# Kernel tuning notes

Hardware: AMD Instinct MI355X
Metric: run time of the kernel (lower is better)

The kernel has to match this reference:

```python
import jax, jax.numpy as jnp
import numpy as np

H = 16  # heads

def setup_inputs() -> dict:
    key = jax.random.key(0)
    k1, k2, k3 = jax.random.split(key, 3)
    B, N, D = 2, 2048, 1024
    x = jax.random.normal(k1, (B, N, D), dtype=jnp.float32)
    W1 = jax.random.normal(k2, (D, 3 * D), dtype=jnp.float32) * (1.0 / np.sqrt(D))
    b1 = jnp.zeros((3 * D,), dtype=jnp.float32)
    W2 = jax.random.normal(k3, (D, D), dtype=jnp.float32) * (1.0 / np.sqrt(D))
    b2 = jnp.zeros((D,), dtype=jnp.float32)
    return {"x": x, "W1": W1, "b1": b1, "W2": W2, "b2": b2}

def reference(x, W1, b1, W2, b2):
    B, N, D = x.shape
    Dh = D // H  # head dim
    qkv = x @ W1 + b1                         # [B,N,3D]
    q, k, v = jnp.split(qkv, 3, axis=-1)
    q = q.reshape(B, N, H, Dh).transpose(0, 2, 1, 3)  # [B,H,N,Dh]
    k = k.reshape(B, N, H, Dh).transpose(0, 2, 1, 3)
    v = v.reshape(B, N, H, Dh).transpose(0, 2, 1, 3)
    scale = 1.0 / np.sqrt(Dh)
    w = jnp.einsum('bhnd,bhmd->bhnm', q, k) * scale   # [B,H,N,N]
    w = jax.nn.softmax(w, axis=-1)
    out = jnp.einsum('bhnm,bhmd->bhnd', w, v)         # [B,H,N,Dh]
    out = out.transpose(0, 2, 1, 3).reshape(B, N, D)
    return out @ W2 + b2
```

## Files before the change

kernel.cpp:

```cpp
#include <hip/hip_runtime.h>
#include <hip/hip_bf16.h>
#include <stdint.h>

#define B_   2
#define H_   16
#define N_   2048
#define D_   1024
#define DH   64
#define MTOK 4096

#define LOG2E 1.44269504088896f

typedef __attribute__((ext_vector_type(8)))  short bf16x8;
typedef __attribute__((ext_vector_type(4)))  float f32x4;
typedef __attribute__((ext_vector_type(16))) float f32x16;
typedef __attribute__((ext_vector_type(2)))  unsigned u32x2;
typedef __attribute__((ext_vector_type(4)))  unsigned short us4;

#define VMCNT_ASM(N) asm volatile("s_waitcnt vmcnt(" #N ")" ::: "memory")

static __device__ __forceinline__ unsigned short f2bf(float f) {
    union { float f; unsigned u; } v; v.f = f;
    unsigned r = v.u + 0x7fffu + ((v.u >> 16) & 1u);
    return (unsigned short)(r >> 16);
}

static __device__ __forceinline__ unsigned f2u(float x) {
    union { float f; unsigned u; } v; v.f = x; return v.u;
}
static __device__ __forceinline__ float u2f(unsigned x) {
    union { unsigned u; float f; } v; v.u = x; return v.f;
}

static __device__ __forceinline__ unsigned cvt_pk_bf16(float lo, float hi) {
    unsigned r;
    asm("v_cvt_pk_bf16_f32 %0, %1, %2" : "=v"(r) : "v"(lo), "v"(hi));
    return r;
}

static __device__ __forceinline__ bf16x8 frag_from_u32(unsigned a, unsigned b, unsigned c, unsigned d) {
    union { unsigned u[4]; bf16x8 v; } x;
    x.u[0] = a; x.u[1] = b; x.u[2] = c; x.u[3] = d;
    return x.v;
}

static __device__ __forceinline__ void load_lds16(const void* g, void* l) {
    __builtin_amdgcn_global_load_lds(
        (const __attribute__((address_space(1))) unsigned int*)g,
        (__attribute__((address_space(3))) unsigned int*)l, 16, 0, 0);
}

__global__ __launch_bounds__(256) void k_cvt_x(const float* __restrict__ x,
                                               unsigned short* __restrict__ xb, int n) {
    int idx = (blockIdx.x * 256 + threadIdx.x) * 4;
    if (idx < n) {
        float4 v = *(const float4*)(x + idx);
        us4 o;
        o.x = f2bf(v.x); o.y = f2bf(v.y); o.z = f2bf(v.z); o.w = f2bf(v.w);
        *(us4*)(xb + idx) = o;
    }
}

__global__ __launch_bounds__(256) void k_transpose_w(const float* __restrict__ in,
                                                     unsigned short* __restrict__ out,
                                                     int R, int C) {
    __shared__ float tile[64][65];
    int c0 = blockIdx.x * 64, r0 = blockIdx.y * 64;
    int t = threadIdx.x;
    int tr = t >> 4, tc = (t & 15) * 4;
#pragma unroll
    for (int p = 0; p < 4; p++) {
        int row = p * 16 + tr;
        float4 v = *(const float4*)(in + (size_t)(r0 + row) * C + c0 + tc);
        tile[row][tc + 0] = v.x; tile[row][tc + 1] = v.y;
        tile[row][tc + 2] = v.z; tile[row][tc + 3] = v.w;
    }
    __syncthreads();
    int oc = t >> 4, orr = (t & 15) * 4;
#pragma unroll
    for (int p = 0; p < 4; p++) {
        int crow = p * 16 + oc;
        us4 o;
        o.x = f2bf(tile[orr + 0][crow]);
        o.y = f2bf(tile[orr + 1][crow]);
        o.z = f2bf(tile[orr + 2][crow]);
        o.w = f2bf(tile[orr + 3][crow]);
        *(us4*)(out + (size_t)(c0 + crow) * R + r0 + orr) = o;
    }
}

__global__ __launch_bounds__(512, 2) void k_gemm0(const unsigned short* __restrict__ A,
                                                  const unsigned short* __restrict__ Bt,
                                                  const float* __restrict__ bias,
                                                  unsigned short* __restrict__ qdst,
                                                  unsigned short* __restrict__ kdst,
                                                  unsigned short* __restrict__ vdst) {
    __shared__ unsigned short lds[57344];
    const int K = 1024, NT = 16;
    int tid = threadIdx.x;
    int lane = tid & 63, wv = tid >> 6;
    int wm = wv >> 2, wn = wv & 3;
    int F = blockIdx.x;
    int L = (F & 7) * 32 + (F >> 3);
    int n0 = (L % 16) * 192;
    int m0 = (L / 16) * 256;

    f32x4 acc[8][3];
#pragma unroll
    for (int i = 0; i < 8; i++)
#pragma unroll
        for (int j = 0; j < 3; j++) {
            f32x4 z; z[0] = 0.f; z[1] = 0.f; z[2] = 0.f; z[3] = 0.f;
            acc[i][j] = z;
        }

    auto stage = [&](int t) {
        int p = t & 1;
        int k0 = t * 64;
        unsigned short* ab = &lds[p * 16384];
        unsigned short* bb = &lds[32768 + p * 12288];
#pragma unroll
        for (int i = 0; i < 4; i++) {
            int u = i * 512 + tid;
            int r = u >> 3, c8 = u & 7;
            int c8s = c8 ^ ((r & 4) ? 2 : 0);
            int db = (i * 512 + wv * 64) * 8;
            load_lds16(A + (size_t)(m0 + r) * K + k0 + c8s * 8, &ab[db]);
            if (i < 3)
                load_lds16(Bt + (size_t)(n0 + r) * K + k0 + c8s * 8, &bb[db]);
        }
    };

    stage(0);
    stage(1);

    const int ml = lane & 15, kl = (lane >> 4) * 8;
    const int cswz = (lane & 4) ? 16 : 0;
    bf16x8 afr[4], bfr[3];

#pragma unroll 1
    for (int t = 0; t < NT; ++t) {
        if (t < NT - 1) { VMCNT_ASM(7); }
        else            { VMCNT_ASM(0); }
        __builtin_amdgcn_s_barrier();

        const unsigned short* ab = &lds[(t & 1) * 16384];
        const unsigned short* bb = &lds[32768 + (t & 1) * 12288];

#pragma unroll
        for (int kk = 0; kk < 2; ++kk) {
            int ck = (kk * 32 + kl) ^ cswz;
#pragma unroll
            for (int mh = 0; mh < 2; ++mh) {
                if (mh == 0) {
#pragma unroll
                    for (int nj = 0; nj < 3; nj++)
                        bfr[nj] = *(const bf16x8*)&bb[(wn * 48 + nj * 16 + ml) * 64 + ck];
                }
#pragma unroll
                for (int q = 0; q < 4; q++)
                    afr[q] = *(const bf16x8*)&ab[(wm * 128 + (mh * 4 + q) * 16 + ml) * 64 + ck];
                __builtin_amdgcn_s_barrier();
                __builtin_amdgcn_s_setprio(1);
#pragma unroll
                for (int q = 0; q < 4; q++)
#pragma unroll
                    for (int nj = 0; nj < 3; nj++)
                        acc[mh * 4 + q][nj] = __builtin_amdgcn_mfma_f32_16x16x32_bf16(
                            afr[q], bfr[nj], acc[mh * 4 + q][nj], 0, 0, 0);
                __builtin_amdgcn_s_setprio(0);
                __builtin_amdgcn_s_barrier();
            }
        }
        if (t + 2 < NT) stage(t + 2);
    }

#pragma unroll
    for (int nj = 0; nj < 3; nj++) {
        int col = n0 + wn * 48 + nj * 16 + (lane & 15);
        float bv = bias[col];
        int which = col >> 10;
        int hd = (col >> 6) & 15;
        int dh = col & 63;
        float scl = (which == 0) ? (0.125f * LOG2E) : 1.0f;
#pragma unroll
        for (int mi = 0; mi < 8; mi++) {
            int rbase = m0 + wm * 128 + mi * 16 + (lane >> 4) * 4;
#pragma unroll
            for (int r = 0; r < 4; r++) {
                int tok = rbase + r;
                int bb2 = tok >> 11, nn = tok & 2047;
                float vvv = (acc[mi][nj][r] + bv) * scl;
                size_t chunk = ((size_t)(bb2 * H_ + hd) * 64 + (nn >> 5)) * 2048;
                if (which == 0) {
                    qdst[((size_t)(bb2 * H_ + hd) * N_ + nn) * DH + dh] = f2bf(vvv);
                } else if (which == 1) {
                    int lane2 = ((dh >> 3) & 1) * 32 + (nn & 31);
                    kdst[chunk + (dh >> 4) * 512 + lane2 * 8 + (dh & 7)] = f2bf(vvv);
                } else {
                    int lane2 = ((nn >> 3) & 1) * 32 + (dh & 31);
                    int islot = (dh >> 5) * 2 + ((nn >> 4) & 1);
                    vdst[chunk + islot * 512 + lane2 * 8 + (nn & 7)] = f2bf(vvv);
                }
            }
        }
    }
}

__global__ __launch_bounds__(256) void k_gemm1(const unsigned short* __restrict__ A,
                                               const unsigned short* __restrict__ Bt,
                                               const float* __restrict__ bias,
                                               float* __restrict__ outp) {
    __shared__ unsigned short As[3][128 * 32];
    __shared__ unsigned short Bs[3][128 * 32];
    const int K = 1024;
    const int NT = 32;
    int tid = threadIdx.x;
    int lane = tid & 63, wv = tid >> 6;
    int wm = wv >> 1, wn = wv & 1;

    const int NX = 8, CPX = 32;
    int F = blockIdx.x;
    int L = (F & 7) * CPX + (F >> 3);
    int n0 = (L % NX) * 128;
    int m0 = (L / NX) * 128;
    int bIdx = m0 >> 11;
    int ntok0 = m0 & 2047;

    f32x4 acc[4][4];
#pragma unroll
    for (int i = 0; i < 4; i++)
#pragma unroll
        for (int j = 0; j < 4; j++) {
            f32x4 z; z[0] = 0.f; z[1] = 0.f; z[2] = 0.f; z[3] = 0.f;
            acc[i][j] = z;
        }

    auto stage = [&](int buf, int tt) {
        int k0 = tt * 32;
        int hh = k0 >> 6;
        const unsigned short* aptr = A + ((size_t)(bIdx * H_ + hh) * N_ + ntok0) * DH + (k0 & 63);
        const unsigned short* bptr = Bt + (size_t)n0 * K + k0;
#pragma unroll
        for (int i = 0; i < 2; i++) {
            int cidb = i * 256 + wv * 64;
            int cid = cidb + lane;
            int row = cid >> 2;
            int cg  = (cid & 3) ^ (row & 3);
            load_lds16(aptr + (size_t)row * DH + cg * 8, &As[buf][cidb * 8]);
            load_lds16(bptr + (size_t)row * K  + cg * 8, &Bs[buf][cidb * 8]);
        }
    };

    stage(0, 0);
    stage(1, 1);

    const int swz = ((lane >> 4) ^ (lane & 3)) * 8;
    const int ar0 = (wm * 64 + (lane & 15)) * 32 + swz;
    const int br0 = (wn * 64 + (lane & 15)) * 32 + swz;

#pragma unroll 1
    for (int t = 0; t < NT; ++t) {
        int cur = t % 3;
        if (t <= NT - 3) stage((t + 2) % 3, t + 2);
        if (t <= NT - 3)      { VMCNT_ASM(8); }
        else if (t == NT - 2) { VMCNT_ASM(4); }
        else                  { VMCNT_ASM(0); }
        __builtin_amdgcn_s_barrier();
        __builtin_amdgcn_sched_barrier(0);

        bf16x8 af[4], bfr[4];
#pragma unroll
        for (int mi = 0; mi < 4; mi++)
            af[mi] = *(const bf16x8*)&As[cur][ar0 + mi * 16 * 32];
#pragma unroll
        for (int ni = 0; ni < 4; ni++)
            bfr[ni] = *(const bf16x8*)&Bs[cur][br0 + ni * 16 * 32];
#pragma unroll
        for (int mi = 0; mi < 4; mi++)
#pragma unroll
            for (int ni = 0; ni < 4; ni++)
                acc[mi][ni] = __builtin_amdgcn_mfma_f32_16x16x32_bf16(
                    af[mi], bfr[ni], acc[mi][ni], 0, 0, 0);

        __builtin_amdgcn_s_barrier();
    }

#pragma unroll
    for (int ni = 0; ni < 4; ni++) {
        int col = n0 + wn * 64 + ni * 16 + (lane & 15);
        float bv = bias[col];
#pragma unroll
        for (int mi = 0; mi < 4; mi++) {
            int rbase = m0 + wm * 64 + mi * 16 + (lane >> 4) * 4;
#pragma unroll
            for (int r = 0; r < 4; r++)
                outp[(size_t)(rbase + r) * D_ + col] = acc[mi][ni][r] + bv;
        }
    }
}

__global__ __launch_bounds__(512, 2) void k_attn(const unsigned short* __restrict__ qh,
                                                 const unsigned short* __restrict__ ks,
                                                 const unsigned short* __restrict__ vs,
                                                 unsigned short* __restrict__ o) {
    __shared__ unsigned short smem[32768];
    unsigned short* kb = smem;
    unsigned short* vb = smem + 16384;
    float* red = (float*)smem;

    int tid = threadIdx.x;
    int lane = tid & 63, wv = tid >> 6;
    int qsub = wv >> 1;
    int kvh  = wv & 1;
    int F = blockIdx.x;
    int L = (F & 7) * 64 + (F >> 3);
    int bh = L >> 4;
    int q0 = (L & 15) * 128 + qsub * 32;
    int ln = lane & 31, hi = lane >> 5;
    const size_t bhO = (size_t)bh * N_ * DH;

    const unsigned short* qp = qh + bhO;
    bf16x8 qf[4];
#pragma unroll
    for (int kk = 0; kk < 4; kk++)
        qf[kk] = *(const bf16x8*)(qp + (size_t)(q0 + ln) * DH + kk * 16 + hi * 8);

    const unsigned short* kg = ks + (size_t)bh * 131072;
    const unsigned short* vg = vs + (size_t)bh * 131072;

    int sbuf = wv >> 1;
    int sl   = wv & 1;
    int sh   = sbuf & 1;
    unsigned short* dstb = ((sbuf >> 1) ? vb : kb) + sh * 8192 + sl * 2048;
    const unsigned short* srcb = ((sbuf >> 1) ? vg : kg) + (size_t)sh * 65536 + sl * 2048;
    auto stageT = [&](int ring, int t) {
#pragma unroll
        for (int i = 0; i < 4; i++)
            load_lds16(srcb + (size_t)t * 4096 + i * 512 + lane * 8,
                       dstb + ring * 4096 + i * 512);
    };

    f32x16 o0, o1;
#pragma unroll
    for (int r = 0; r < 16; r++) { o0[r] = 0.f; o1[r] = 0.f; }
    float m = -INFINITY, l = 0.f;

    stageT(0, 0);
    __syncthreads();

#pragma unroll 1
    for (int t = 0; t < 16; ++t) {
        int b = t & 1;
        if (t < 15) stageT(b ^ 1, t + 1);

        const unsigned short* kB = kb + kvh * 8192 + b * 4096;
        const unsigned short* vB = vb + kvh * 8192 + b * 4096;

        bf16x8 kfa[4], kfb[4];
#pragma unroll
        for (int i = 0; i < 4; i++) {
            kfa[i] = *(const bf16x8*)&kB[i * 512 + lane * 8];
            kfb[i] = *(const bf16x8*)&kB[2048 + i * 512 + lane * 8];
        }
        f32x16 sa, sb;
#pragma unroll
        for (int r = 0; r < 16; r++) { sa[r] = 0.f; sb[r] = 0.f; }
#pragma unroll
        for (int i = 0; i < 4; i++)
            sa = __builtin_amdgcn_mfma_f32_32x32x16_bf16(kfa[i], qf[i], sa, 0, 0, 0);
#pragma unroll
        for (int i = 0; i < 4; i++)
            sb = __builtin_amdgcn_mfma_f32_32x32x16_bf16(kfb[i], qf[i], sb, 0, 0, 0);

        float mx[8];
#pragma unroll
        for (int i = 0; i < 8; i++)
            mx[i] = fmaxf(fmaxf(sa[i], sa[i + 8]), fmaxf(sb[i], sb[i + 8]));
#pragma unroll
        for (int i = 0; i < 4; i++) mx[i] = fmaxf(mx[i], mx[i + 4]);
        float mt = fmaxf(fmaxf(mx[0], mx[2]), fmaxf(mx[1], mx[3]));
        {
            u32x2 sw = __builtin_amdgcn_permlane32_swap(f2u(mt), f2u(mt), false, false);
            mt = fmaxf(u2f(sw[0]), u2f(sw[1]));
        }
        if (!__all(mt <= m + 8.0f)) {
            float mn = fmaxf(m, mt);
            float fs = __builtin_amdgcn_exp2f(m - mn);
            m = mn;
            l *= fs;
#pragma unroll
            for (int r = 0; r < 16; r++) { o0[r] *= fs; o1[r] *= fs; }
        }
        float pa[16], pb[16];
#pragma unroll
        for (int r = 0; r < 16; r++) {
            pa[r] = __builtin_amdgcn_exp2f(sa[r] - m);
            pb[r] = __builtin_amdgcn_exp2f(sb[r] - m);
        }
        float sm[8];
#pragma unroll
        for (int i = 0; i < 8; i++) sm[i] = (pa[i] + pa[i + 8]) + (pb[i] + pb[i + 8]);
#pragma unroll
        for (int i = 0; i < 4; i++) sm[i] = sm[i] + sm[i + 4];
        float sum = (sm[0] + sm[2]) + (sm[1] + sm[3]);
        {
            u32x2 sw = __builtin_amdgcn_permlane32_swap(f2u(sum), f2u(sum), false, false);
            sum = u2f(sw[0]) + u2f(sw[1]);
        }
        l += sum;

        unsigned pka[8], pkb[8];
#pragma unroll
        for (int i = 0; i < 8; i++) {
            pka[i] = cvt_pk_bf16(pa[2 * i], pa[2 * i + 1]);
            pkb[i] = cvt_pk_bf16(pb[2 * i], pb[2 * i + 1]);
        }
        u32x2 s0 = __builtin_amdgcn_permlane32_swap(pka[0], pka[2], false, false);
        u32x2 s1 = __builtin_amdgcn_permlane32_swap(pka[1], pka[3], false, false);
        u32x2 s2 = __builtin_amdgcn_permlane32_swap(pka[4], pka[6], false, false);
        u32x2 s3 = __builtin_amdgcn_permlane32_swap(pka[5], pka[7], false, false);
        bf16x8 pf0 = frag_from_u32(s0[0], s1[0], s0[1], s1[1]);
        bf16x8 pf1 = frag_from_u32(s2[0], s3[0], s2[1], s3[1]);
        s0 = __builtin_amdgcn_permlane32_swap(pkb[0], pkb[2], false, false);
        s1 = __builtin_amdgcn_permlane32_swap(pkb[1], pkb[3], false, false);
        s2 = __builtin_amdgcn_permlane32_swap(pkb[4], pkb[6], false, false);
        s3 = __builtin_amdgcn_permlane32_swap(pkb[5], pkb[7], false, false);
        bf16x8 pf2 = frag_from_u32(s0[0], s1[0], s0[1], s1[1]);
        bf16x8 pf3 = frag_from_u32(s2[0], s3[0], s2[1], s3[1]);

        bf16x8 vf0, vf1, vf2, vf3;
        vf0 = *(const bf16x8*)&vB[0 * 512 + lane * 8];
        vf1 = *(const bf16x8*)&vB[1 * 512 + lane * 8];
        vf2 = *(const bf16x8*)&vB[2048 + 0 * 512 + lane * 8];
        vf3 = *(const bf16x8*)&vB[2048 + 1 * 512 + lane * 8];
        o0 = __builtin_amdgcn_mfma_f32_32x32x16_bf16(vf0, pf0, o0, 0, 0, 0);
        o0 = __builtin_amdgcn_mfma_f32_32x32x16_bf16(vf1, pf1, o0, 0, 0, 0);
        o0 = __builtin_amdgcn_mfma_f32_32x32x16_bf16(vf2, pf2, o0, 0, 0, 0);
        o0 = __builtin_amdgcn_mfma_f32_32x32x16_bf16(vf3, pf3, o0, 0, 0, 0);
        vf0 = *(const bf16x8*)&vB[2 * 512 + lane * 8];
        vf1 = *(const bf16x8*)&vB[3 * 512 + lane * 8];
        vf2 = *(const bf16x8*)&vB[2048 + 2 * 512 + lane * 8];
        vf3 = *(const bf16x8*)&vB[2048 + 3 * 512 + lane * 8];
        o1 = __builtin_amdgcn_mfma_f32_32x32x16_bf16(vf0, pf0, o1, 0, 0, 0);
        o1 = __builtin_amdgcn_mfma_f32_32x32x16_bf16(vf1, pf1, o1, 0, 0, 0);
        o1 = __builtin_amdgcn_mfma_f32_32x32x16_bf16(vf2, pf2, o1, 0, 0, 0);
        o1 = __builtin_amdgcn_mfma_f32_32x32x16_bf16(vf3, pf3, o1, 0, 0, 0);

        __syncthreads();
    }

    if (kvh == 1) {
        float* rp = red + (qsub * 64 + lane) * 34;
#pragma unroll
        for (int r = 0; r < 16; r++) { rp[r] = o0[r]; rp[16 + r] = o1[r]; }
        rp[32] = m;
        rp[33] = l;
    }
    __syncthreads();
    if (kvh == 0) {
        const float* rp = red + (qsub * 64 + lane) * 34;
        float mb = rp[32], lb = rp[33];
        float mn = fmaxf(m, mb);
        float fa = __builtin_amdgcn_exp2f(m - mn);
        float fb = __builtin_amdgcn_exp2f(mb - mn);
        float inv = 1.0f / (l * fa + lb * fb);
        float ga = fa * inv, gb = fb * inv;
        unsigned short* ob = o + bhO + (size_t)(q0 + ln) * DH;
#pragma unroll
        for (int t2 = 0; t2 < 2; t2++) {
#pragma unroll
            for (int g = 0; g < 4; g++) {
                int d = t2 * 32 + g * 8 + hi * 4;
                int rb = g * 4;
                float a0 = (t2 ? o1[rb + 0] : o0[rb + 0]) * ga + rp[t2 * 16 + rb + 0] * gb;
                float a1 = (t2 ? o1[rb + 1] : o0[rb + 1]) * ga + rp[t2 * 16 + rb + 1] * gb;
                float a2 = (t2 ? o1[rb + 2] : o0[rb + 2]) * ga + rp[t2 * 16 + rb + 2] * gb;
                float a3 = (t2 ? o1[rb + 3] : o0[rb + 3]) * ga + rp[t2 * 16 + rb + 3] * gb;
                us4 w;
                w.x = f2bf(a0); w.y = f2bf(a1); w.z = f2bf(a2); w.w = f2bf(a3);
                *(us4*)(ob + d) = w;
            }
        }
    }
}

extern "C" void kernel_launch(void* const* d_in, const int* in_sizes, int n_in,
                              void* d_out, int out_size, void* d_ws, size_t ws_size,
                              hipStream_t stream) {
    const float* x  = (const float*)d_in[0];
    const float* W1 = (const float*)d_in[1];
    const float* b1 = (const float*)d_in[2];
    const float* W2 = (const float*)d_in[3];
    const float* b2 = (const float*)d_in[4];
    float* out = (float*)d_out;

    char* ws = (char*)d_ws;
    unsigned short* xb   = (unsigned short*)(ws);
    unsigned short* w1t  = (unsigned short*)(ws + 8388608);
    unsigned short* w2t  = (unsigned short*)(ws + 14680064);
    unsigned short* qh   = (unsigned short*)(ws + 16777216);
    unsigned short* ks   = (unsigned short*)(ws + 25165824);
    unsigned short* vsb  = (unsigned short*)(ws + 33554432);
    unsigned short* attn = (unsigned short*)(ws + 41943040);

    k_cvt_x<<<4096, 256, 0, stream>>>(x, xb, MTOK * D_);
    k_transpose_w<<<dim3(48, 16), 256, 0, stream>>>(W1, w1t, D_, 3 * D_);
    k_transpose_w<<<dim3(16, 16), 256, 0, stream>>>(W2, w2t, D_, D_);
    k_gemm0<<<256, 512, 0, stream>>>(xb, w1t, b1, qh, ks, vsb);
    k_attn<<<512, 512, 0, stream>>>(qh, ks, vsb, attn);
    k_gemm1<<<256, 256, 0, stream>>>(attn, w2t, b2, out);
}
```

Measured before the change: 125.4 us.

## Merge preprocessing kernels, use full XOR LDS swizzle, raise MFMA priority

Folds the x conversion and both weight transposes into one launch that picks its role from the block index, removing two kernel launches and their gaps. Changes the gemm0 LDS swizzle from a 2-bit pattern to a full row&7 XOR so fragment reads spread across more LDS banks. Wraps the attention MFMA groups in s_setprio raise/lower so waves issuing matrix ops get scheduling priority. The fused pre-kernel adds branch divergence per block, and the swizzle must match between the global-to-LDS stores and the fragment reads.

```diff
diff --git a/kernel.cpp b/kernel.cpp
--- a/kernel.cpp
+++ b/kernel.cpp
@@ -50,23 +50,30 @@
         (__attribute__((address_space(3))) unsigned int*)l, 16, 0, 0);
 }
 
-__global__ __launch_bounds__(256) void k_cvt_x(const float* __restrict__ x,
-                                               unsigned short* __restrict__ xb, int n) {
-    int idx = (blockIdx.x * 256 + threadIdx.x) * 4;
-    if (idx < n) {
+__global__ __launch_bounds__(256) void k_pre(const float* __restrict__ x,
+                                             unsigned short* __restrict__ xb,
+                                             const float* __restrict__ W1,
+                                             unsigned short* __restrict__ w1t,
+                                             const float* __restrict__ W2,
+                                             unsigned short* __restrict__ w2t) {
+    int blk = blockIdx.x;
+    int t = threadIdx.x;
+    if (blk < 4096) {
+        int idx = (blk * 256 + t) * 4;
         float4 v = *(const float4*)(x + idx);
         us4 o;
         o.x = f2bf(v.x); o.y = f2bf(v.y); o.z = f2bf(v.z); o.w = f2bf(v.w);
         *(us4*)(xb + idx) = o;
-    }
-}
-
-__global__ __launch_bounds__(256) void k_transpose_w(const float* __restrict__ in,
-                                                     unsigned short* __restrict__ out,
-                                                     int R, int C) {
+        return;
+    }
+    const float* in;
+    unsigned short* out;
+    int C, bx, by;
+    if (blk < 4864) { in = W1; out = w1t; C = 3072; int b2 = blk - 4096; bx = b2 % 48; by = b2 / 48; }
+    else            { in = W2; out = w2t; C = 1024; int b2 = blk - 4864; bx = b2 % 16; by = b2 / 16; }
+    const int R = 1024;
     __shared__ float tile[64][65];
-    int c0 = blockIdx.x * 64, r0 = blockIdx.y * 64;
-    int t = threadIdx.x;
+    int c0 = bx * 64, r0 = by * 64;
     int tr = t >> 4, tc = (t & 15) * 4;
 #pragma unroll
     for (int p = 0; p < 4; p++) {
@@ -123,7 +130,7 @@
         for (int i = 0; i < 4; i++) {
             int u = i * 512 + tid;
             int r = u >> 3, c8 = u & 7;
-            int c8s = c8 ^ ((r & 4) ? 2 : 0);
+            int c8s = c8 ^ (r & 7);
             int db = (i * 512 + wv * 64) * 8;
             load_lds16(A + (size_t)(m0 + r) * K + k0 + c8s * 8, &ab[db]);
             if (i < 3)
@@ -134,8 +141,7 @@
     stage(0);
     stage(1);
 
-    const int ml = lane & 15, kl = (lane >> 4) * 8;
-    const int cswz = (lane & 4) ? 16 : 0;
+    const int ml = lane & 15, ul = lane >> 4;
     bf16x8 afr[4], bfr[3];
 
 #pragma unroll 1
@@ -149,7 +155,7 @@
 
 #pragma unroll
         for (int kk = 0; kk < 2; ++kk) {
-            int ck = (kk * 32 + kl) ^ cswz;
+            int ck = ((kk * 4 + ul) ^ (ml & 7)) * 8;
 #pragma unroll
             for (int mh = 0; mh < 2; ++mh) {
                 if (mh == 0) {
@@ -366,12 +372,14 @@
         f32x16 sa, sb;
 #pragma unroll
         for (int r = 0; r < 16; r++) { sa[r] = 0.f; sb[r] = 0.f; }
+        __builtin_amdgcn_s_setprio(1);
 #pragma unroll
         for (int i = 0; i < 4; i++)
             sa = __builtin_amdgcn_mfma_f32_32x32x16_bf16(kfa[i], qf[i], sa, 0, 0, 0);
 #pragma unroll
         for (int i = 0; i < 4; i++)
             sb = __builtin_amdgcn_mfma_f32_32x32x16_bf16(kfb[i], qf[i], sb, 0, 0, 0);
+        __builtin_amdgcn_s_setprio(0);
 
         float mx[8];
 #pragma unroll
@@ -434,18 +442,22 @@
         vf1 = *(const bf16x8*)&vB[1 * 512 + lane * 8];
         vf2 = *(const bf16x8*)&vB[2048 + 0 * 512 + lane * 8];
         vf3 = *(const bf16x8*)&vB[2048 + 1 * 512 + lane * 8];
+        __builtin_amdgcn_s_setprio(1);
         o0 = __builtin_amdgcn_mfma_f32_32x32x16_bf16(vf0, pf0, o0, 0, 0, 0);
         o0 = __builtin_amdgcn_mfma_f32_32x32x16_bf16(vf1, pf1, o0, 0, 0, 0);
         o0 = __builtin_amdgcn_mfma_f32_32x32x16_bf16(vf2, pf2, o0, 0, 0, 0);
         o0 = __builtin_amdgcn_mfma_f32_32x32x16_bf16(vf3, pf3, o0, 0, 0, 0);
+        __builtin_amdgcn_s_setprio(0);
         vf0 = *(const bf16x8*)&vB[2 * 512 + lane * 8];
         vf1 = *(const bf16x8*)&vB[3 * 512 + lane * 8];
         vf2 = *(const bf16x8*)&vB[2048 + 2 * 512 + lane * 8];
         vf3 = *(const bf16x8*)&vB[2048 + 3 * 512 + lane * 8];
+        __builtin_amdgcn_s_setprio(1);
         o1 = __builtin_amdgcn_mfma_f32_32x32x16_bf16(vf0, pf0, o1, 0, 0, 0);
         o1 = __builtin_amdgcn_mfma_f32_32x32x16_bf16(vf1, pf1, o1, 0, 0, 0);
         o1 = __builtin_amdgcn_mfma_f32_32x32x16_bf16(vf2, pf2, o1, 0, 0, 0);
         o1 = __builtin_amdgcn_mfma_f32_32x32x16_bf16(vf3, pf3, o1, 0, 0, 0);
+        __builtin_amdgcn_s_setprio(0);
 
         __syncthreads();
     }
@@ -504,9 +516,7 @@
     unsigned short* vsb  = (unsigned short*)(ws + 33554432);
     unsigned short* attn = (unsigned short*)(ws + 41943040);
 
-    k_cvt_x<<<4096, 256, 0, stream>>>(x, xb, MTOK * D_);
-    k_transpose_w<<<dim3(48, 16), 256, 0, stream>>>(W1, w1t, D_, 3 * D_);
-    k_transpose_w<<<dim3(16, 16), 256, 0, stream>>>(W2, w2t, D_, D_);
+    k_pre<<<5120, 256, 0, stream>>>(x, xb, W1, w1t, W2, w2t);
     k_gemm0<<<256, 512, 0, stream>>>(xb, w1t, b1, qh, ks, vsb);
     k_attn<<<512, 512, 0, stream>>>(qh, ks, vsb, attn);
     k_gemm1<<<256, 256, 0, stream>>>(attn, w2t, b2, out);
```

Result: faster. 119.9 us (-4.4%).
